# Optimization experiments

Measured on AMD Instinct MI355X. Metric: run time of the kernel, lower is better.

## Reference

```python
import jax, jax.numpy as jnp
import numpy as np


def conv1x1(x, w, b):
    # 1x1 conv == channel contraction: w [O,I], x [B,I,H,W] -> [B,O,H,W]
    return jnp.einsum('oi,bihw->bohw', w, x) + b[None, :, None, None]


def inorm(x, eps):
    # InstanceNorm2d (no affine): normalize per-sample per-channel over spatial dims
    m = jnp.mean(x, axis=(2, 3), keepdims=True)
    v = jnp.var(x, axis=(2, 3), keepdims=True)
    return (x - m) * jax.lax.rsqrt(v + eps)


def bnorm(x, eps=1e-5):
    # BatchNorm2d in training mode with weight=1, bias=0: batch stats over (B,H,W)
    m = jnp.mean(x, axis=(0, 2, 3), keepdims=True)
    v = jnp.var(x, axis=(0, 2, 3), keepdims=True)
    return (x - m) * jax.lax.rsqrt(v + eps)


def setup_inputs() -> dict:
    key = jax.random.key(0)
    ks = jax.random.split(key, 12)
    B, N, K, Ci, Co = 16, 2000, 9, 256, 128
    s = 0.05
    return {
        'x_row': jax.random.normal(ks[0], (B, Co, N, 1), jnp.float32),
        'x_local': jax.random.normal(ks[1], (B, Ci, N, K), jnp.float32),
        'w_att1': jax.random.normal(ks[2], (Co, Ci), jnp.float32) * s,
        'b_att1': jnp.zeros((Co,), jnp.float32),
        'wq': jax.random.normal(ks[3], (Co, Co), jnp.float32) * s,
        'bq': jnp.zeros((Co,), jnp.float32),
        'wk': jax.random.normal(ks[4], (Co, Co), jnp.float32) * s,
        'bk': jnp.zeros((Co,), jnp.float32),
        'wv': jax.random.normal(ks[5], (Co, Co), jnp.float32) * s,
        'bv': jnp.zeros((Co,), jnp.float32),
        'w_right': jax.random.normal(ks[6], (Co, Ci), jnp.float32) * s,
        'b_right': jnp.zeros((Co,), jnp.float32),
        'w_l1': jax.random.normal(ks[7], (Co, Ci), jnp.float32) * s,
        'b_l1': jnp.zeros((Co,), jnp.float32),
        'w_l2': jax.random.normal(ks[8], (Co, Co), jnp.float32) * s,
        'b_l2': jnp.zeros((Co,), jnp.float32),
        'w_l3': jax.random.normal(ks[9], (Co, Co), jnp.float32) * s,
        'b_l3': jnp.zeros((Co,), jnp.float32),
        'gamma1': jnp.ones((1,), jnp.float32),
    }


def reference(x_row, x_local, w_att1, b_att1, wq, bq, wk, bk, wv, bv,
              w_right, b_right, w_l1, b_l1, w_l2, b_l2, w_l3, b_l3, gamma1):
    # att1: InstanceNorm(eps=1e-3) -> BatchNorm -> ReLU -> 1x1 conv
    xl = conv1x1(jax.nn.relu(bnorm(inorm(x_local, 1e-3))), w_att1, b_att1)
    q = conv1x1(x_row, wq, bq)      # [B,C,N,1]
    k = conv1x1(xl, wk, bk)         # [B,C,N,K]
    v = conv1x1(xl, wv, bv)         # [B,C,N,K]
    att = jax.nn.softmax(q * k, axis=3)             # broadcast q over K
    out_local = jnp.sum(att * v, axis=3, keepdims=True)  # [B,C,N,1]
    h = jnp.concatenate([x_row, out_local], axis=1)      # [B,2C,N,1]
    # ResNet_Block(pre=True): right branch is 1x1 conv shortcut
    x1 = conv1x1(h, w_right, b_right)
    o1 = jax.nn.relu(bnorm(inorm(conv1x1(h, w_l1, b_l1), 1e-5))) + x1
    o2 = jax.nn.relu(bnorm(inorm(conv1x1(o1, w_l2, b_l2), 1e-5))) + o1 + x1
    o3 = jax.nn.relu(bnorm(inorm(conv1x1(o2, w_l3, b_l3), 1e-5)) + x1)
    out = x_row + gamma1 * o3
    return (out + out.mean(axis=1, keepdims=True)) * 0.5
```

## Files before the change

kernel.cpp:

```cpp
#include <hip/hip_runtime.h>
#include <math.h>

#define NB    16
#define CIx   256
#define COx   128
#define NPTS  2000
#define KW    9
#define NKx   18000
#define NTIL  25
#define PSTRIDE 51200

typedef short bf16x8 __attribute__((ext_vector_type(8)));
typedef float f32x4  __attribute__((ext_vector_type(4)));

__device__ __forceinline__ ushort f2bf(float f){
  unsigned u = __builtin_bit_cast(unsigned, f);
  u = (u + 0x7fffu + ((u>>16)&1u)) >> 16;
  return (ushort)u;
}
__device__ __forceinline__ float bf2f(ushort h){
  unsigned u = ((unsigned)h)<<16;
  return __builtin_bit_cast(float, u);
}
__device__ __forceinline__ int pi16(int c, int mt){
  return (((c & 3) ^ (mt & 3)) << 2) | (c >> 2);
}

__global__ __launch_bounds__(256) void k_xstats(const float* __restrict__ xl,
    float* __restrict__ sum, float* __restrict__ sumsq){
  int bi = blockIdx.x;
  const float4* p = (const float4*)(xl + (size_t)bi * NKx);
  float s = 0.f, ss = 0.f;
  for (int idx = threadIdx.x; idx < NKx/4; idx += 256){
    float4 v = p[idx];
    s  += v.x + v.y + v.z + v.w;
    ss += v.x*v.x + v.y*v.y + v.z*v.z + v.w*v.w;
  }
  __shared__ float rs[256], rss[256];
  rs[threadIdx.x] = s; rss[threadIdx.x] = ss;
  __syncthreads();
  for (int off = 128; off > 0; off >>= 1){
    if (threadIdx.x < off){ rs[threadIdx.x] += rs[threadIdx.x+off]; rss[threadIdx.x] += rss[threadIdx.x+off]; }
    __syncthreads();
  }
  if (threadIdx.x == 0){ sum[bi] = rs[0]; sumsq[bi] = rss[0]; }
}

__global__ void k_xscale(const float* __restrict__ sum, const float* __restrict__ sumsq,
                         float* __restrict__ mOut, float* __restrict__ sOut){
  int i = threadIdx.x;
  float vl[NB], ml[NB];
  float V = 0.f;
  for (int b = 0; b < NB; b++){
    int bi = b*CIx + i;
    float m = sum[bi] * (1.f/(float)NKx);
    float v = sumsq[bi] * (1.f/(float)NKx) - m*m;
    ml[b] = m; vl[b] = v;
    V += v / (v + 1e-3f);
  }
  V *= (1.f/(float)NB);
  float bs = rsqrtf(V + 1e-5f);
  for (int b = 0; b < NB; b++){
    int bi = b*CIx + i;
    mOut[bi] = ml[b];
    sOut[bi] = rsqrtf(vl[b] + 1e-3f) * bs;
  }
}

__global__ void k_prep_kv(const float* __restrict__ w_att1, const float* __restrict__ wk,
                          const float* __restrict__ wv, const float* __restrict__ b_att1,
                          const float* __restrict__ bk, const float* __restrict__ bv,
                          ushort* __restrict__ Wf, float* __restrict__ bKV){
  int r = blockIdx.x;
  int i = threadIdx.x;
  const float* wr = (r < 128) ? (wk + r*128) : (wv + (r-128)*128);
  float acc = 0.f;
  for (int c = 0; c < 128; c++) acc += wr[c] * w_att1[c*CIx + i];
  Wf[r*256 + i] = f2bf(acc);
  if (i == 0){
    float bacc = (r < 128) ? bk[r] : bv[r-128];
    for (int c = 0; c < 128; c++) bacc += wr[c] * b_att1[c];
    bKV[r] = bacc;
  }
}

__global__ void k_prepW(const float* __restrict__ wq, const float* __restrict__ w_right,
                        const float* __restrict__ w_l1, const float* __restrict__ w_l2,
                        const float* __restrict__ w_l3, const float* __restrict__ b_right,
                        const float* __restrict__ b_l1,
                        ushort* __restrict__ Wq, ushort* __restrict__ W2,
                        ushort* __restrict__ W3, ushort* __restrict__ W4,
                        float* __restrict__ bias2){
  int idx = blockIdx.x*256 + threadIdx.x;
  if (idx < 16384){ Wq[idx] = f2bf(wq[idx]); return; }
  idx -= 16384;
  if (idx < 65536){
    int r = idx >> 8, i = idx & 255;
    W2[idx] = f2bf(r < 128 ? w_right[r*256+i] : w_l1[(r-128)*256+i]);
    return;
  }
  idx -= 65536;
  if (idx < 16384){ W3[idx] = f2bf(w_l2[idx]); return; }
  idx -= 16384;
  if (idx < 16384){ W4[idx] = f2bf(w_l3[idx]); return; }
  idx -= 16384;
  if (idx < 256) bias2[idx] = (idx < 128) ? b_right[idx] : b_l1[idx-128];
}

__global__ __launch_bounds__(256,3) void k_attn_mfma(
    const float* __restrict__ xl,
    const float* __restrict__ mArr, const float* __restrict__ sArr,
    const ushort* __restrict__ Wf, const float* __restrict__ bKV,
    const float* __restrict__ Pq,
    float* __restrict__ out_local)
{
  const int b   = blockIdx.y;
  const int n0  = blockIdx.x * 8;
  const int col0 = n0 * KW;
  const int tid = threadIdx.x;
  const int w   = tid >> 6;
  const int lane = tid & 63;
  const int c16 = lane & 15, g = lane >> 4;

  __shared__ ushort wlds[20480];
  ushort (*elds)[16][72] = (ushort (*)[16][72])wlds;
  float* obuf = (float*)(wlds + 18432);

  {
    unsigned* fb = (unsigned*)wlds;
#pragma unroll
    for (int zz = 0; zz < 4; zz++){
      int z = tid + 256*zz;
      int io2 = z & 3, cj = 8 + ((z>>2)&7), g_ = (z>>5)&3, s = z>>7;
      fb[((s*5 + 4)*4 + g_)*64 + pi16(cj,4)*4 + io2] = 0u;
    }
  }

  {
    const size_t xb = (size_t)b*CIx*NKx + col0;
    const float* mB = mArr + b*CIx;
    const float* sB = sArr + b*CIx;
#pragma unroll
    for (int kk = 0; kk < 9; kk++){
      int idx = tid + 256*kk;
      int il  = idx / 18;
      int c4  = idx - 18*il;
      int i_l = 2*il;
      int col = 4*c4;
      const float* gp = xl + xb + (size_t)i_l*NKx + col;
      float4 ra = *(const float4*)gp;
      float4 rb = *(const float4*)(gp + NKx);
      float2 mm = *(const float2*)(mB + i_l);
      float2 ssv = *(const float2*)(sB + i_l);
      int s = i_l >> 5, g_ = (i_l >> 3) & 3, io2 = il & 3;
      int mt = c4 >> 2;
      unsigned* dstb = (unsigned*)wlds + ((s*5 + mt)*4 + g_)*64 + io2;
      float a0[4] = {ra.x, ra.y, ra.z, ra.w};
      float a1[4] = {rb.x, rb.y, rb.z, rb.w};
#pragma unroll
      for (int j = 0; j < 4; j++){
        int cj = (col + j) & 15;
        float v0 = fmaxf((a0[j] - mm.x)*ssv.x, 0.f);
        float v1 = fmaxf((a1[j] - mm.y)*ssv.y, 0.f);
        dstb[pi16(cj, mt)*4] = (unsigned)f2bf(v0) | ((unsigned)f2bf(v1) << 16);
      }
    }
  }
  __syncthreads();

  f32x4 acc[5][4];
#pragma unroll
  for (int mt = 0; mt < 5; mt++)
#pragma unroll
    for (int j = 0; j < 4; j++) acc[mt][j] = (f32x4)0.f;

  {
    const int ct0 = w, ct1 = w + 4, ct2 = w + 8, ct3 = w + 12;
#pragma unroll
    for (int s = 0; s < 8; s++){
      bf16x8 wf0 = *(const bf16x8*)(Wf + (ct0*16 + c16)*256 + s*32 + g*8);
      bf16x8 wf1 = *(const bf16x8*)(Wf + (ct1*16 + c16)*256 + s*32 + g*8);
      bf16x8 wf2 = *(const bf16x8*)(Wf + (ct2*16 + c16)*256 + s*32 + g*8);
      bf16x8 wf3 = *(const bf16x8*)(Wf + (ct3*16 + c16)*256 + s*32 + g*8);
#pragma unroll
      for (int mt = 0; mt < 5; mt++){
        bf16x8 af = *(const bf16x8*)(wlds + ((s*5 + mt)*4 + g)*128 + pi16(c16, mt)*8);
        acc[mt][0] = __builtin_amdgcn_mfma_f32_16x16x32_bf16(af, wf0, acc[mt][0], 0,0,0);
        acc[mt][1] = __builtin_amdgcn_mfma_f32_16x16x32_bf16(af, wf1, acc[mt][1], 0,0,0);
        acc[mt][2] = __builtin_amdgcn_mfma_f32_16x16x32_bf16(af, wf2, acc[mt][2], 0,0,0);
        acc[mt][3] = __builtin_amdgcn_mfma_f32_16x16x32_bf16(af, wf3, acc[mt][3], 0,0,0);
      }
    }
  }
  __syncthreads();

  const int chA = w*16 + c16;
  float2 qa, qb;
  {
    const float* p0 = Pq + ((size_t)(b*COx + chA))*NPTS + n0 + 2*g;
    qa = *(const float2*)p0;
    qb = *(const float2*)(p0 + 64*NPTS);
  }
  float bk0 = bKV[chA], bk1 = bKV[chA + 64];
  float bv0 = bKV[128 + chA], bv1 = bKV[128 + chA + 64];

#pragma unroll
  for (int mt = 0; mt < 5; mt++){
    if (mt < 4 || g < 2){
      int colb = 16*mt + 4*g;
#pragma unroll
      for (int j = 0; j < 4; j++){
#pragma unroll
        for (int r2 = 0; r2 < 2; r2++){
          unsigned pk = (unsigned)f2bf(acc[mt][j][2*r2]) | ((unsigned)f2bf(acc[mt][j][2*r2+1]) << 16);
          *(unsigned*)&elds[w*4 + j][c16][colb + 2*r2] = pk;
        }
      }
    }
  }
  __syncthreads();

#pragma unroll
  for (int h = 0; h < 2; h++){
    float bk_ = h ? bk1 : bk0;
    float bv_ = h ? bv1 : bv0;
    int ch = chA + 64*h;
    const ushort* eK = &elds[w*4 + h][c16][0];
    const ushort* eV = &elds[w*4 + 2 + h][c16][0];
#pragma unroll
    for (int t = 0; t < 2; t++){
      int nloc = 2*g + t;
      int cb = 9*nloc;
      float qq = h ? (t ? qb.y : qb.x) : (t ? qa.y : qa.x);
      float sc[KW];
      float mx = -1e30f;
#pragma unroll
      for (int k = 0; k < KW; k++){
        float s_ = qq * (bf2f(eK[cb + k]) + bk_);
        sc[k] = s_;
        mx = fmaxf(mx, s_);
      }
      float den = 0.f, num = 0.f;
#pragma unroll
      for (int k = 0; k < KW; k++){
        float e = __expf(sc[k] - mx);
        den += e;
        num += e * (bf2f(eV[cb + k]) + bv_);
      }
      obuf[ch*8 + nloc] = num / den;
    }
  }
  __syncthreads();

  {
    int ch = tid >> 1, part = tid & 1;
    float4 v = *(float4*)&obuf[ch*8 + 4*part];
    *(float4*)(out_local + ((size_t)(b*COx + ch))*NPTS + n0 + 4*part) = v;
  }
}

template<int MODE>
__global__ __launch_bounds__(256) void k_mconv(
    const float* __restrict__ inA, const float* __restrict__ inB,
    const ushort* __restrict__ Wc, const float* __restrict__ bias,
    const float* __restrict__ nm, const float* __restrict__ nsc,
    float* __restrict__ out0, float* __restrict__ out1,
    float* __restrict__ uout, float* __restrict__ pstat)
{
  constexpr int IC = (MODE==1) ? 256 : 128;
  constexpr int RC = (MODE==1) ? 256 : 128;
  constexpr int NS = IC/32;
  constexpr int JW = RC/64;
  constexpr int PHASES = RC/128;
  constexpr bool STATS = (MODE >= 1);
  constexpr int SPH = (MODE==1) ? 1 : 0;

  const int b = blockIdx.y, bx = blockIdx.x;
  const int n0 = bx*80;
  const int tid = threadIdx.x;
  const int w = tid>>6, lane = tid&63;
  const int c16 = lane&15, g = lane>>4;

  __shared__ ushort smem[21504];

  {
    constexpr int TOT = (IC/2)*20;
    const float* srcA = inA + (size_t)b*128*NPTS;
    const float* srcB = inB ? (inB + (size_t)b*128*NPTS) : nullptr;
    for (int idx = tid; idx < TOT; idx += 256){
      int pr = idx/20, c4 = idx - 20*pr;
      int i = pr*2;
      int cc = n0 + 4*c4;
      float4 va, vb;
      if (MODE == 0){
        const float* base = srcA + (size_t)i*NPTS + cc;
        va = *(const float4*)base;
        vb = *(const float4*)(base + NPTS);
      } else if (MODE == 1){
        const float* base = (i < 128) ? (srcA + (size_t)i*NPTS + cc)
                                      : (srcB + (size_t)(i-128)*NPTS + cc);
        va = *(const float4*)base;
        vb = *(const float4*)(base + NPTS);
      } else {
        const float* pa = srcA + (size_t)i*NPTS + cc;
        const float* pb = srcB + (size_t)i*NPTS + cc;
        float4 ca = *(const float4*)pa, cb = *(const float4*)(pa+NPTS);
        float4 aa = *(const float4*)pb, ab = *(const float4*)(pb+NPTS);
        float m0 = nm[b*128+i],   s0 = nsc[b*128+i];
        float m1 = nm[b*128+i+1], s1 = nsc[b*128+i+1];
        va.x = fmaxf((ca.x-m0)*s0,0.f)+aa.x; va.y = fmaxf((ca.y-m0)*s0,0.f)+aa.y;
        va.z = fmaxf((ca.z-m0)*s0,0.f)+aa.z; va.w = fmaxf((ca.w-m0)*s0,0.f)+aa.w;
        vb.x = fmaxf((cb.x-m1)*s1,0.f)+ab.x; vb.y = fmaxf((cb.y-m1)*s1,0.f)+ab.y;
        vb.z = fmaxf((cb.z-m1)*s1,0.f)+ab.z; vb.w = fmaxf((cb.w-m1)*s1,0.f)+ab.w;
        if (MODE == 2){
          float4 u0, u1;
          u0.x = va.x+aa.x; u0.y = va.y+aa.y; u0.z = va.z+aa.z; u0.w = va.w+aa.w;
          u1.x = vb.x+ab.x; u1.y = vb.y+ab.y; u1.z = vb.z+ab.z; u1.w = vb.w+ab.w;
          *(float4*)(uout + ((size_t)(b*128+i))*NPTS + cc) = u0;
          *(float4*)(uout + ((size_t)(b*128+i+1))*NPTS + cc) = u1;
        }
      }
      int sp = i>>5, g_ = (i>>3)&3, io2 = (i>>1)&3;
      int mt = c4>>2;
      unsigned* dstb = (unsigned*)smem + ((sp*5 + mt)*4 + g_)*64 + io2;
      float a0[4] = {va.x, va.y, va.z, va.w};
      float a1[4] = {vb.x, vb.y, vb.z, vb.w};
#pragma unroll
      for (int j = 0; j < 4; j++){
        int cj = (4*c4 + j) & 15;
        int pi = pi16(cj, mt);
        dstb[pi*4] = (unsigned)f2bf(a0[j]) | ((unsigned)f2bf(a1[j]) << 16);
      }
    }
  }
  __syncthreads();

  f32x4 acc[5][JW];
#pragma unroll
  for (int mt = 0; mt < 5; mt++)
#pragma unroll
    for (int j = 0; j < JW; j++) acc[mt][j] = (f32x4)0.f;

  for (int s = 0; s < NS; s++){
    bf16x8 wf[JW];
#pragma unroll
    for (int j = 0; j < JW; j++)
      wf[j] = *(const bf16x8*)(Wc + ((w + 4*j)*16 + c16)*IC + s*32 + g*8);
#pragma unroll
    for (int mt = 0; mt < 5; mt++){
      bf16x8 af = *(const bf16x8*)(smem + ((s*5 + mt)*4 + g)*128 + pi16(c16, mt)*8);
#pragma unroll
      for (int j = 0; j < JW; j++)
        acc[mt][j] = __builtin_amdgcn_mfma_f32_16x16x32_bf16(af, wf[j], acc[mt][j], 0,0,0);
    }
  }

  float* dl = (float*)smem;
#pragma unroll
  for (int ph = 0; ph < PHASES; ph++){
    __syncthreads();
    float st_s[2], st_ss[2];
#pragma unroll
    for (int jj = 0; jj < 2; jj++){
      int j = ph*2 + jj;
      int ct = w + 4*j;
      int rl = (ct & 7)*16 + c16;
      float bb = bias[ct*16 + c16];
      float s = 0.f, ss = 0.f;
#pragma unroll
      for (int mt = 0; mt < 5; mt++){
        f32x4 v = acc[mt][j];
        float4 vv;
        vv.x = v[0]+bb; vv.y = v[1]+bb; vv.z = v[2]+bb; vv.w = v[3]+bb;
        *(float4*)&dl[rl*84 + mt*16 + 4*g] = vv;
        s  += vv.x + vv.y + vv.z + vv.w;
        ss += vv.x*vv.x + vv.y*vv.y + vv.z*vv.z + vv.w*vv.w;
      }
      st_s[jj] = s; st_ss[jj] = ss;
    }
    if (STATS && ph == SPH){
#pragma unroll
      for (int jj = 0; jj < 2; jj++){
        float s = st_s[jj], ss = st_ss[jj];
        s += __shfl_xor(s, 16); ss += __shfl_xor(ss, 16);
        s += __shfl_xor(s, 32); ss += __shfl_xor(ss, 32);
        if (g == 0){
          int ct = w + 4*(ph*2 + jj);
          int rl = (ct & 7)*16 + c16;
          int off = (b*NTIL + bx)*128 + rl;
          pstat[off]           = s;
          pstat[PSTRIDE + off] = ss;
        }
      }
    }
    __syncthreads();
    float* dst = ph ? out1 : out0;
#pragma unroll
    for (int kk = 0; kk < 10; kk++){
      int idx = kk*256 + tid;
      int r = idx/20, c4 = idx - 20*r;
      *(float4*)(dst + ((size_t)(b*128 + r))*NPTS + n0 + 4*c4) = *(float4*)&dl[r*84 + 4*c4];
    }
  }
}

__global__ __launch_bounds__(1024) void k_red(const float* __restrict__ pstat,
                                              float* __restrict__ cm, float* __restrict__ cs){
  __shared__ float msh[2048], vsh[2048], wsh[2048];
  int t = threadIdx.x;
#pragma unroll
  for (int h = 0; h < 2; h++){
    int p = t + h*1024;
    int b = p >> 7, c = p & 127;
    float s = 0.f, ss = 0.f;
    for (int tt = 0; tt < NTIL; tt++){
      int off = (b*NTIL + tt)*128 + c;
      s  += pstat[off];
      ss += pstat[PSTRIDE + off];
    }
    float m = s * (1.f/(float)NPTS);
    float v = ss * (1.f/(float)NPTS) - m*m;
    msh[p] = m; vsh[p] = v; wsh[p] = v/(v + 1e-5f);
  }
  __syncthreads();
  if (t < 128){
    float V = 0.f;
    for (int b = 0; b < NB; b++) V += wsh[b*128 + t];
    float bs = rsqrtf(V*(1.f/(float)NB) + 1e-5f);
    for (int b = 0; b < NB; b++){
      cm[b*COx + t] = msh[b*128 + t];
      cs[b*COx + t] = rsqrtf(vsh[b*128 + t] + 1e-5f) * bs;
    }
  }
}

__global__ __launch_bounds__(256) void k_final(const float* __restrict__ c3, const float* __restrict__ x1,
    const float* __restrict__ x_row, const float* __restrict__ cm, const float* __restrict__ cs,
    const float* __restrict__ gamma1, float* __restrict__ out)
{
  const int b  = blockIdx.y;
  const int n0 = blockIdx.x * 50;
  const int tid = threadIdx.x;
  const float g = gamma1[0];
  __shared__ float tt[128][50];
  __shared__ float part[4][50];
  for (int idx = tid; idx < 128*50; idx += 256){
    int c = idx / 50; int j = idx - c*50;
    size_t off = ((size_t)b*COx + c)*NPTS + n0 + j;
    float o3 = fmaxf((c3[off] - cm[b*COx + c]) * cs[b*COx + c] + x1[off], 0.f);
    tt[c][j] = x_row[off] + g * o3;
  }
  __syncthreads();
  if (tid < 200){
    int gg = tid / 50, j = tid - gg*50;
    float s = 0.f;
    for (int c = gg*32; c < gg*32 + 32; c++) s += tt[c][j];
    part[gg][j] = s;
  }
  __syncthreads();
  for (int idx = tid; idx < 128*50; idx += 256){
    int c = idx / 50; int j = idx - c*50;
    float mean = (part[0][j] + part[1][j] + part[2][j] + part[3][j]) * (1.f/128.f);
    out[((size_t)b*COx + c)*NPTS + n0 + j] = 0.5f * (tt[c][j] + mean);
  }
}

extern "C" void kernel_launch(void* const* d_in, const int* in_sizes, int n_in,
                              void* d_out, int out_size, void* d_ws, size_t ws_size,
                              hipStream_t stream){
  (void)in_sizes; (void)n_in; (void)out_size; (void)ws_size;
  const float* x_row   = (const float*)d_in[0];
  const float* x_local = (const float*)d_in[1];
  const float* w_att1  = (const float*)d_in[2];
  const float* b_att1  = (const float*)d_in[3];
  const float* wq      = (const float*)d_in[4];
  const float* bq      = (const float*)d_in[5];
  const float* wk      = (const float*)d_in[6];
  const float* bk      = (const float*)d_in[7];
  const float* wv      = (const float*)d_in[8];
  const float* bv      = (const float*)d_in[9];
  const float* w_right = (const float*)d_in[10];
  const float* b_right = (const float*)d_in[11];
  const float* w_l1    = (const float*)d_in[12];
  const float* b_l1    = (const float*)d_in[13];
  const float* w_l2    = (const float*)d_in[14];
  const float* b_l2    = (const float*)d_in[15];
  const float* w_l3    = (const float*)d_in[16];
  const float* b_l3    = (const float*)d_in[17];
  const float* gamma1  = (const float*)d_in[18];
  float* out = (float*)d_out;

  float*  ws     = (float*)d_ws;
  float*  sum    = ws;
  float*  sumsq  = ws + 4096;
  float*  mArr   = ws + 8192;
  float*  sArr   = ws + 12288;
  ushort* Wf     = (ushort*)(ws + 16384);
  float*  bKV    = ws + 49152;
  ushort* Wq     = (ushort*)(ws + 49408);
  ushort* W2     = (ushort*)(ws + 57600);
  ushort* W3     = (ushort*)(ws + 90368);
  ushort* W4     = (ushort*)(ws + 98560);
  float*  bias2  = ws + 106752;
  float*  cm     = ws + 107008;
  float*  cs     = ws + 109056;
  float*  pstat  = ws + 111104;
  float*  P0 = ws + 262144;
  float*  P1 = P0 + 4096000;
  float*  P2 = P1 + 4096000;
  float*  P3 = P2 + 4096000;

  k_xstats <<<4096, 256, 0, stream>>>(x_local, sum, sumsq);
  k_xscale <<<1, 256, 0, stream>>>(sum, sumsq, mArr, sArr);
  k_prep_kv<<<256, 256, 0, stream>>>(w_att1, wk, wv, b_att1, bk, bv, Wf, bKV);
  k_prepW  <<<450, 256, 0, stream>>>(wq, w_right, w_l1, w_l2, w_l3, b_right, b_l1,
                                     Wq, W2, W3, W4, bias2);

  k_mconv<0><<<dim3(NTIL, NB), 256, 0, stream>>>(x_row, nullptr, Wq, bq,
                                                 nullptr, nullptr, P1, nullptr, nullptr, nullptr);

  k_attn_mfma<<<dim3(250, NB), 256, 0, stream>>>(x_local, mArr, sArr, Wf, bKV, P1, P0);

  k_mconv<1><<<dim3(NTIL, NB), 256, 0, stream>>>(x_row, P0, W2, bias2,
                                                 nullptr, nullptr, P1, P2, nullptr, pstat);
  k_red<<<1, 1024, 0, stream>>>(pstat, cm, cs);

  k_mconv<2><<<dim3(NTIL, NB), 256, 0, stream>>>(P2, P1, W3, b_l2,
                                                 cm, cs, P3, nullptr, P0, pstat);
  k_red<<<1, 1024, 0, stream>>>(pstat, cm, cs);

  k_mconv<3><<<dim3(NTIL, NB), 256, 0, stream>>>(P3, P0, W4, b_l3,
                                                 cm, cs, P2, nullptr, nullptr, pstat);
  k_red<<<1, 1024, 0, stream>>>(pstat, cm, cs);

  k_final<<<dim3(NPTS/50, NB), 256, 0, stream>>>(P2, P1, x_row, cm, cs, gamma1, out);
}
```

Measured before the change: 311.8 us.

## Fuse query projection into attention kernel via MFMA, drop separate q conv launch

Computes the q = Wq·x_row projection inside the attention kernel with bf16 MFMA on an 8-point tile staged in LDS, instead of launching a separate k_mconv<0> pass that writes q to global memory and reading it back. This removes one kernel launch and a full round trip of the q tensor through global memory. In exchange it adds extra LDS and a few MFMAs per block, which could lower occupancy of the attention kernel.

```diff
diff --git a/kernel.cpp b/kernel.cpp
--- a/kernel.cpp
+++ b/kernel.cpp
@@ -108,10 +108,10 @@
 }
 
 __global__ __launch_bounds__(256,3) void k_attn_mfma(
-    const float* __restrict__ xl,
+    const float* __restrict__ xl, const float* __restrict__ x_row,
     const float* __restrict__ mArr, const float* __restrict__ sArr,
     const ushort* __restrict__ Wf, const float* __restrict__ bKV,
-    const float* __restrict__ Pq,
+    const ushort* __restrict__ Wq, const float* __restrict__ bq,
     float* __restrict__ out_local)
 {
   const int b   = blockIdx.y;
@@ -123,6 +123,8 @@
   const int c16 = lane & 15, g = lane >> 4;
 
   __shared__ ushort wlds[20480];
+  __shared__ ushort qlds[2048];
+  __shared__ float  qbuf[128*8];
   ushort (*elds)[16][72] = (ushort (*)[16][72])wlds;
   float* obuf = (float*)(wlds + 18432);
 
@@ -133,6 +135,20 @@
       int z = tid + 256*zz;
       int io2 = z & 3, cj = 8 + ((z>>2)&7), g_ = (z>>5)&3, s = z>>7;
       fb[((s*5 + 4)*4 + g_)*64 + pi16(cj,4)*4 + io2] = 0u;
+    }
+  }
+
+  {
+    int row = tid >> 1, half = tid & 1;
+    const float* xr = x_row + ((size_t)(b*COx + row))*NPTS + n0 + 4*half;
+    float4 v = *(const float4*)xr;
+    int kq = row >> 5, g_ = (row >> 3) & 3, io = row & 7;
+    int base = (kq*4 + g_)*128 + io;
+    float a[4] = {v.x, v.y, v.z, v.w};
+#pragma unroll
+    for (int j = 0; j < 4; j++){
+      qlds[base + (4*half + j)*8] = f2bf(a[j]);
+      qlds[base + (8 + 4*half + j)*8] = 0;
     }
   }
 
@@ -192,18 +208,33 @@
       }
     }
   }
+
+  f32x4 accq[2];
+  accq[0] = (f32x4)0.f; accq[1] = (f32x4)0.f;
+  {
+#pragma unroll
+    for (int kq = 0; kq < 4; kq++){
+      bf16x8 afq = *(const bf16x8*)(qlds + (kq*4 + g)*128 + c16*8);
+      bf16x8 wq0 = *(const bf16x8*)(Wq + ((w     )*16 + c16)*128 + kq*32 + g*8);
+      bf16x8 wq1 = *(const bf16x8*)(Wq + ((w + 4 )*16 + c16)*128 + kq*32 + g*8);
+      accq[0] = __builtin_amdgcn_mfma_f32_16x16x32_bf16(afq, wq0, accq[0], 0,0,0);
+      accq[1] = __builtin_amdgcn_mfma_f32_16x16x32_bf16(afq, wq1, accq[1], 0,0,0);
+    }
+  }
   __syncthreads();
 
   const int chA = w*16 + c16;
-  float2 qa, qb;
-  {
-    const float* p0 = Pq + ((size_t)(b*COx + chA))*NPTS + n0 + 2*g;
-    qa = *(const float2*)p0;
-    qb = *(const float2*)(p0 + 64*NPTS);
-  }
-  float bk0 = bKV[chA], bk1 = bKV[chA + 64];
-  float bv0 = bKV[128 + chA], bv1 = bKV[128 + chA + 64];
-
+
+  if (g < 2){
+#pragma unroll
+    for (int j = 0; j < 2; j++){
+      int ch = chA + 64*j;
+      float bb = bq[ch];
+#pragma unroll
+      for (int r2 = 0; r2 < 4; r2++)
+        qbuf[ch*8 + 4*g + r2] = accq[j][r2] + bb;
+    }
+  }
 #pragma unroll
   for (int mt = 0; mt < 5; mt++){
     if (mt < 4 || g < 2){
@@ -219,6 +250,9 @@
     }
   }
   __syncthreads();
+
+  float bk0 = bKV[chA], bk1 = bKV[chA + 64];
+  float bv0 = bKV[128 + chA], bv1 = bKV[128 + chA + 64];
 
 #pragma unroll
   for (int h = 0; h < 2; h++){
@@ -231,7 +265,7 @@
     for (int t = 0; t < 2; t++){
       int nloc = 2*g + t;
       int cb = 9*nloc;
-      float qq = h ? (t ? qb.y : qb.x) : (t ? qa.y : qa.x);
+      float qq = qbuf[ch*8 + nloc];
       float sc[KW];
       float mx = -1e30f;
 #pragma unroll
@@ -292,11 +326,7 @@
       int i = pr*2;
       int cc = n0 + 4*c4;
       float4 va, vb;
-      if (MODE == 0){
-        const float* base = srcA + (size_t)i*NPTS + cc;
-        va = *(const float4*)base;
-        vb = *(const float4*)(base + NPTS);
-      } else if (MODE == 1){
+      if (MODE == 1){
         const float* base = (i < 128) ? (srcA + (size_t)i*NPTS + cc)
                                       : (srcB + (size_t)(i-128)*NPTS + cc);
         va = *(const float4*)base;
@@ -516,10 +546,7 @@
   k_prepW  <<<450, 256, 0, stream>>>(wq, w_right, w_l1, w_l2, w_l3, b_right, b_l1,
                                      Wq, W2, W3, W4, bias2);
 
-  k_mconv<0><<<dim3(NTIL, NB), 256, 0, stream>>>(x_row, nullptr, Wq, bq,
-                                                 nullptr, nullptr, P1, nullptr, nullptr, nullptr);
-
-  k_attn_mfma<<<dim3(250, NB), 256, 0, stream>>>(x_local, mArr, sArr, Wf, bKV, P1, P0);
+  k_attn_mfma<<<dim3(250, NB), 256, 0, stream>>>(x_local, x_row, mArr, sArr, Wf, bKV, Wq, bq, P0);
 
   k_mconv<1><<<dim3(NTIL, NB), 256, 0, stream>>>(x_row, P0, W2, bias2,
                                                  nullptr, nullptr, P1, P2, nullptr, pstat);
```

Measured after the change: 310.3 us. No clear change (-0.5%).
